# Optimization experiments

Measured on AMD Instinct MI355X. Metric: run time of the kernel, lower is better.

## Reference

```python
import jax, jax.numpy as jnp
import numpy as np

B, D, K = 32768, 256, 2048
BETA = 0.25


def setup_inputs() -> dict:
    key = jax.random.key(0)
    k1, k2 = jax.random.split(key)
    latents = jax.random.normal(k1, (B, D), dtype=jnp.float32)
    # nn.Embedding weight initialized uniform(-1/K, 1/K)
    embedding = jax.random.uniform(k2, (K, D), dtype=jnp.float32,
                                   minval=-1.0 / K, maxval=1.0 / K)
    return {"latents": latents, "embedding": embedding}


def reference(latents, embedding):
    # Squared-L2 distances: [B, K]
    dist = (jnp.sum(latents ** 2, axis=1, keepdims=True)
            + jnp.sum(embedding ** 2, axis=1)
            - 2.0 * jnp.matmul(latents, embedding.T))
    encoding_inds = jnp.argmin(dist, axis=1)  # [B]

    # Gather codebook rows (equivalent to one-hot @ embedding)
    quantized = embedding[encoding_inds]  # [B, D]

    commitment_loss = jnp.mean((jax.lax.stop_gradient(quantized) - latents) ** 2)
    embedding_loss = jnp.mean((quantized - jax.lax.stop_gradient(latents)) ** 2)
    vq_loss = commitment_loss * BETA + embedding_loss

    # Straight-through estimator
    quantized_st = latents + jax.lax.stop_gradient(quantized - latents)

    # avg_probs = mean of one-hot over batch == normalized histogram of inds
    counts = jnp.zeros((K,), dtype=jnp.float32).at[encoding_inds].add(1.0)
    avg_probs = counts / B
    entropy_vq = -jnp.sum(avg_probs * jnp.log(avg_probs + 1e-10))

    # dist values at selected codes
    cluster_metric = jnp.mean(
        jnp.take_along_axis(dist, encoding_inds[:, None], axis=1))

    return (quantized_st, vq_loss, entropy_vq,
            encoding_inds[:, None], cluster_metric)
```

## Files before the change

### kernel.cpp

```cpp
#include <hip/hip_runtime.h>
#include <math.h>

#define B_ROWS 32768
#define D_DIM  256
#define K_CODES 2048

#define OUT_Q   0
#define OUT_VQ  8388608
#define OUT_ENT 8388609
#define OUT_IND 8388610
#define OUT_CM  8421378


#define WS_SE2   0
#define WS_SX2   8192
#define WS_CNT   139264
#define WS_PACK  147456
#define WS_MSEP  409600
#define WS_DISTP 475136
#define WS_BCAT  540672

typedef _Float16 f16x8 __attribute__((ext_vector_type(8)));
typedef float f32x4 __attribute__((ext_vector_type(4)));
typedef union { _Float16 h[4]; uint2 u2; } h4pack;

__global__ __launch_bounds__(256) void k_init(
    const float* __restrict__ X, const float* __restrict__ E,
    _Float16* __restrict__ A, _Float16* __restrict__ Bc,
    float* __restrict__ sx2, float* __restrict__ se2,
    unsigned long long* __restrict__ packed, int* __restrict__ counts) {
  int w = threadIdx.x >> 6, lane = threadIdx.x & 63;
  if (blockIdx.x < 8192) {
    int row = blockIdx.x * 4 + w;
    float4 v = ((const float4*)(X + (size_t)row * D_DIM))[lane];
    float s = v.x * v.x + v.y * v.y + v.z * v.z + v.w * v.w;
#pragma unroll
    for (int off = 32; off > 0; off >>= 1) s += __shfl_xor(s, off, 64);
    if (lane == 0) { sx2[row] = s; packed[row] = ~0ull; }
    h4pack hi, lo;
    hi.h[0] = (_Float16)v.x; hi.h[1] = (_Float16)v.y;
    hi.h[2] = (_Float16)v.z; hi.h[3] = (_Float16)v.w;
    lo.h[0] = (_Float16)((v.x - (float)hi.h[0]) * 4096.0f);
    lo.h[1] = (_Float16)((v.y - (float)hi.h[1]) * 4096.0f);
    lo.h[2] = (_Float16)((v.z - (float)hi.h[2]) * 4096.0f);
    lo.h[3] = (_Float16)((v.w - (float)hi.h[3]) * 4096.0f);
    *(uint2*)&A[(size_t)row * 512 + 4 * lane] = hi.u2;
    *(uint2*)&A[(size_t)row * 512 + 256 + 4 * lane] = lo.u2;
  } else {
    int bb = blockIdx.x - 8192;
    int row = bb * 4 + w;
    if (threadIdx.x < 4) counts[bb * 4 + threadIdx.x] = 0;
    float4 v = ((const float4*)(E + (size_t)row * D_DIM))[lane];
    float s = v.x * v.x + v.y * v.y + v.z * v.z + v.w * v.w;
#pragma unroll
    for (int off = 32; off > 0; off >>= 1) s += __shfl_xor(s, off, 64);
    if (lane == 0) se2[row] = s;
    const float S = 4194304.0f;
    const float SH = 0.000244140625f;
    float e0 = v.x * S, e1 = v.y * S, e2 = v.z * S, e3 = v.w * S;
    h4pack b1, b2, b3;
    b1.h[0] = (_Float16)e0; b1.h[1] = (_Float16)e1;
    b1.h[2] = (_Float16)e2; b1.h[3] = (_Float16)e3;
    b2.h[0] = (_Float16)((float)b1.h[0] * SH);
    b2.h[1] = (_Float16)((float)b1.h[1] * SH);
    b2.h[2] = (_Float16)((float)b1.h[2] * SH);
    b2.h[3] = (_Float16)((float)b1.h[3] * SH);
    b3.h[0] = (_Float16)(e0 - (float)b1.h[0]);
    b3.h[1] = (_Float16)(e1 - (float)b1.h[1]);
    b3.h[2] = (_Float16)(e2 - (float)b1.h[2]);
    b3.h[3] = (_Float16)(e3 - (float)b1.h[3]);
    *(uint2*)&Bc[(size_t)row * 768 + 4 * lane] = b1.u2;
    *(uint2*)&Bc[(size_t)row * 768 + 256 + 4 * lane] = b2.u2;
    *(uint2*)&Bc[(size_t)row * 768 + 512 + 4 * lane] = b3.u2;
  }
}

#define BAR()  __builtin_amdgcn_s_barrier()
#define SB0()  __builtin_amdgcn_sched_barrier(0)
#define WLGKM(n)                                                 \
  do {                                                           \
    asm volatile("s_waitcnt lgkmcnt(" #n ")" ::: "memory");      \
    SB0();                                                       \
  } while (0)
#define DSR(dst, a, o) \
  asm volatile("ds_read_b128 %0, %1 offset:" o : "=v"(dst) : "v"(a))

#define MFMA_QUAD(I0, J0, AF, BF)                                            \
  do {                                                                       \
    __builtin_amdgcn_s_setprio(1);                                           \
    _Pragma("unroll") for (int kk = 0; kk < 2; ++kk) {                       \
      _Pragma("unroll") for (int ii = 0; ii < 4; ++ii) {                     \
        _Pragma("unroll") for (int jj = 0; jj < 2; ++jj) {                   \
          acc[(I0) + ii][(J0) + jj] =                                        \
              __builtin_amdgcn_mfma_f32_16x16x32_f16(                        \
                  (AF)[ii * 2 + kk], (BF)[jj * 2 + kk],                      \
                  acc[(I0) + ii][(J0) + jj], 0, 0, 0);                       \
        }                                                                    \
      }                                                                      \
    }                                                                        \
    __builtin_amdgcn_s_setprio(0);                                           \
  } while (0)

__global__ __launch_bounds__(512, 2) void k_mfma2(
    const _Float16* __restrict__ A, const _Float16* __restrict__ Bc,
    const float* __restrict__ se2, const float* __restrict__ sx2,
    unsigned long long* __restrict__ packed) {
  extern __shared__ char smem[];
  const int tid = threadIdx.x;
  const int w = tid >> 6, lane = tid & 63;
  const int wm = w >> 2, wn = w & 3;
  const int q = lane >> 4, c = lane & 15;
  const int rowb = blockIdx.x & 127, colb = blockIdx.x >> 7;
  const int rowpan = rowb * 256, colpan = colb * 256;
  const int rsel = lane >> 3;
  const int chunkb = ((lane & 7) ^ rsel) * 16;
  const int rswz = c & 7;

  const char* Abase = (const char*)A;
  const char* Bbase = (const char*)Bc;

  auto issue = [&](int tt, int g, int bsel) {
    const int hh = (g == 3 || g == 4 || g == 5 || g == 7) ? 1 : 0;
    const int ss = (g == 2 || g == 4 || g == 6 || g == 7) ? 1 : 0;
    const int rl = hh * 128 + ss * 64 + w * 8 + rsel;
    const char* src;
    char* dst;
    if (g == 0 || g >= 5) {
      int aoff = (tt & 3) * 128 + (((tt >> 2) == 1) ? 512 : 0);
      src = Abase + ((size_t)(rowpan + rl) << 10) + aoff + chunkb;
      dst = smem + bsel * 32768 + hh * 16384 + ss * 8192 + w * 1024;
    } else {
      src = Bbase + (size_t)(colpan + rl) * 1536 + tt * 128 + chunkb;
      dst = smem + 65536 + bsel * 32768 + hh * 16384 + ss * 8192 + w * 1024;
    }
    __builtin_amdgcn_global_load_lds(
        (const __attribute__((address_space(1))) unsigned int*)src,
        (__attribute__((address_space(3))) unsigned int*)dst, 16, 0, 0);
  };

  f32x4 acc[8][4];
#pragma unroll
  for (int i = 0; i < 8; ++i)
#pragma unroll
    for (int j = 0; j < 4; ++j) acc[i][j] = (f32x4){0.f, 0.f, 0.f, 0.f};

  const unsigned ldsA = (unsigned)(uintptr_t)smem + (unsigned)((wm * 128 + c) * 128);
  const unsigned ldsB = (unsigned)(uintptr_t)smem + 65536u +
                        (unsigned)((wn * 64 + c) * 128);
  const unsigned sl0 = (unsigned)(((0 * 4 + q) ^ rswz) * 16);
  const unsigned sl1 = (unsigned)(((1 * 4 + q) ^ rswz) * 16);

#pragma unroll
  for (int g = 0; g < 8; ++g) issue(0, g, 0);
  asm volatile("s_waitcnt vmcnt(0)" ::: "memory");
  BAR();

  f16x8 af[8], bf01[4], bf23[4];

#pragma unroll 2
  for (int t = 0; t < 12; ++t) {
    const int bsel = t & 1;
    const bool pre = (t < 11);
    const unsigned aA0 = ldsA + (unsigned)(bsel * 32768) + sl0;
    const unsigned aA1 = ldsA + (unsigned)(bsel * 32768) + sl1;
    const unsigned aB0 = ldsB + (unsigned)(bsel * 32768) + sl0;
    const unsigned aB1 = ldsB + (unsigned)(bsel * 32768) + sl1;

    if (pre) {
#pragma unroll
      for (int g = 0; g < 8; ++g) issue(t + 1, g, bsel ^ 1);
    }

    DSR(af[0], aA0, "0");    DSR(af[1], aA1, "0");
    DSR(af[2], aA0, "2048"); DSR(af[3], aA1, "2048");
    DSR(af[4], aA0, "4096"); DSR(af[5], aA1, "4096");
    DSR(af[6], aA0, "6144"); DSR(af[7], aA1, "6144");
    DSR(bf01[0], aB0, "0");    DSR(bf01[1], aB1, "0");
    DSR(bf01[2], aB0, "2048"); DSR(bf01[3], aB1, "2048");
    DSR(bf23[0], aB0, "4096"); DSR(bf23[1], aB1, "4096");
    DSR(bf23[2], aB0, "6144"); DSR(bf23[3], aB1, "6144");

    WLGKM(4);
    MFMA_QUAD(0, 0, af, bf01);
    WLGKM(0);
    MFMA_QUAD(0, 2, af, bf23);

    DSR(af[0], aA0, "8192");  DSR(af[1], aA1, "8192");
    DSR(af[2], aA0, "10240"); DSR(af[3], aA1, "10240");
    DSR(af[4], aA0, "12288"); DSR(af[5], aA1, "12288");
    DSR(af[6], aA0, "14336"); DSR(af[7], aA1, "14336");
    WLGKM(0);
    MFMA_QUAD(4, 2, af, bf23);
    MFMA_QUAD(4, 0, af, bf01);

    if (pre) {
      asm volatile("s_waitcnt vmcnt(0)" ::: "memory");
      BAR();
    }
  }

  __syncthreads();

  const float inv = 4.76837158203125e-07f;
  float se_j[4];
#pragma unroll
  for (int j = 0; j < 4; ++j) se_j[j] = se2[colpan + wn * 64 + j * 16 + c];
  unsigned long long* m = (unsigned long long*)smem;
#pragma unroll
  for (int i = 0; i < 8; ++i) {
    float4 sx4 = *(const float4*)&sx2[rowpan + wm * 128 + i * 16 + q * 4];
#pragma unroll
    for (int r = 0; r < 4; ++r) {
      float sx = ((const float*)&sx4)[r];
      float bs = 3.402823466e38f;
      int bk = 0;
#pragma unroll
      for (int j = 0; j < 4; ++j) {
        float t1 = sx + se_j[j];
        float d = t1 - acc[i][j][r] * inv;
        if (d < bs) { bs = d; bk = colpan + wn * 64 + j * 16 + c; }
      }
#pragma unroll
      for (int off = 1; off < 16; off <<= 1) {
        float os = __shfl_xor(bs, off, 64);
        int ok = __shfl_xor(bk, off, 64);
        if (os < bs || (os == bs && ok < bk)) { bs = os; bk = ok; }
      }
      if (c == 0) {
        m[wn * 256 + wm * 128 + i * 16 + q * 4 + r] =
            ((unsigned long long)__float_as_uint(bs) << 32) |
            (unsigned long long)(unsigned int)bk;
      }
    }
  }
  __syncthreads();
  if (tid < 256) {
    unsigned long long v = m[tid];
#pragma unroll
    for (int mm = 1; mm < 4; ++mm) {
      unsigned long long o = m[mm * 256 + tid];
      if (o < v) v = o;
    }
    atomicMin(&packed[rowpan + tid], v);
  }
}

__global__ __launch_bounds__(256) void k_gather(
    const float* __restrict__ X, const float* __restrict__ E,
    const unsigned long long* __restrict__ packed, float* __restrict__ outq,
    float* __restrict__ out_ind, int* __restrict__ counts,
    double* __restrict__ msep, double* __restrict__ distp) {
  __shared__ int sk[16];
  __shared__ float sd[16];
  int tid = threadIdx.x;
  if (tid < 16) {
    int row = blockIdx.x * 16 + tid;
    unsigned long long v = packed[row];
    int k = (int)(v & 0xFFFFFFFFull);
    sk[tid] = k;
    sd[tid] = __uint_as_float((unsigned int)(v >> 32));
    out_ind[row] = (float)k;
    atomicAdd(&counts[k], 1);
  }
  __syncthreads();
  int wave = tid >> 6, lane = tid & 63;
  double msum = 0.0, dsum = 0.0;
#pragma unroll
  for (int rr = 0; rr < 4; rr++) {
    int li = wave * 4 + rr;
    int b = blockIdx.x * 16 + li;
    int ind = sk[li];
    float4 x4 = ((const float4*)(X + (size_t)b * D_DIM))[lane];
    float4 q4 = ((const float4*)(E + (size_t)ind * D_DIM))[lane];
    float d0 = q4.x - x4.x, d1 = q4.y - x4.y, d2 = q4.z - x4.z, d3 = q4.w - x4.w;
    float4 o;
    o.x = x4.x + d0; o.y = x4.y + d1; o.z = x4.z + d2; o.w = x4.w + d3;
    ((float4*)(outq + (size_t)b * D_DIM))[lane] = o;
    float v = d0 * d0 + d1 * d1 + d2 * d2 + d3 * d3;
#pragma unroll
    for (int off = 32; off > 0; off >>= 1) v += __shfl_xor(v, off, 64);
    if (lane == 0) { msum += (double)v; dsum += (double)sd[li]; }
  }
  if (lane == 0) {
    int wg = blockIdx.x * 4 + wave;
    msep[wg] = msum;
    distp[wg] = dsum;
  }
}

__global__ __launch_bounds__(256) void k_final(
    const int* __restrict__ counts, const double* __restrict__ msep,
    const double* __restrict__ distp, float* __restrict__ out) {
  __shared__ double red[256];
  int t = threadIdx.x;

  double m = 0.0;
  for (int i = t; i < 8192; i += 256) m += msep[i];
  red[t] = m;
  __syncthreads();
  for (int s = 128; s > 0; s >>= 1) {
    if (t < s) red[t] += red[t + s];
    __syncthreads();
  }
  if (t == 0) {
    double mse = red[0] / ((double)B_ROWS * (double)D_DIM);
    out[OUT_VQ] = (float)(mse * 1.25);
  }
  __syncthreads();

  double d = 0.0;
  for (int i = t; i < 8192; i += 256) d += distp[i];
  red[t] = d;
  __syncthreads();
  for (int s = 128; s > 0; s >>= 1) {
    if (t < s) red[t] += red[t + s];
    __syncthreads();
  }
  if (t == 0) out[OUT_CM] = (float)(red[0] / (double)B_ROWS);
  __syncthreads();

  double e = 0.0;
  for (int k = t; k < K_CODES; k += 256) {
    float p = (float)counts[k] * (1.0f / 32768.0f);
    e += (double)(p * logf(p + 1e-10f));
  }
  red[t] = e;
  __syncthreads();
  for (int s = 128; s > 0; s >>= 1) {
    if (t < s) red[t] += red[t + s];
    __syncthreads();
  }
  if (t == 0) out[OUT_ENT] = (float)(-red[0]);
}

extern "C" void kernel_launch(void* const* d_in, const int* in_sizes, int n_in,
                              void* d_out, int out_size, void* d_ws,
                              size_t ws_size, hipStream_t stream) {
  const float* X = (const float*)d_in[0];
  const float* E = (const float*)d_in[1];
  float* out = (float*)d_out;
  char* ws = (char*)d_ws;
  float* se2 = (float*)(ws + WS_SE2);
  float* sx2 = (float*)(ws + WS_SX2);
  int* counts = (int*)(ws + WS_CNT);
  unsigned long long* packed = (unsigned long long*)(ws + WS_PACK);
  double* msep = (double*)(ws + WS_MSEP);
  double* distp = (double*)(ws + WS_DISTP);
  _Float16* Bcat = (_Float16*)(ws + WS_BCAT);
  _Float16* Acat = (_Float16*)d_out;

  static bool attr_done = false;
  if (!attr_done) {
    hipFuncSetAttribute((const void*)k_mfma2,
                        hipFuncAttributeMaxDynamicSharedMemorySize, 131072);
    attr_done = true;
  }

  k_init<<<8704, 256, 0, stream>>>(X, E, Acat, Bcat, sx2, se2, packed, counts);
  k_mfma2<<<1024, 512, 131072, stream>>>(Acat, Bcat, se2, sx2, packed);
  k_gather<<<B_ROWS / 16, 256, 0, stream>>>(X, E, packed, out + OUT_Q,
                                            out + OUT_IND, counts, msep, distp);
  k_final<<<1, 256, 0, stream>>>(counts, msep, distp, out);
}
```

Before: 261.2 us.

## Batch row loads in init and gather kernels; drop MFMA priority toggles

The init kernel now has each wave handle four rows and issues all four global loads before any compute, cutting the grid from 8704 to 2176 blocks. The gather kernel likewise hoists all X and codebook-row loads ahead of the arithmetic so more memory requests are in flight at once. Inside the MFMA main loop the s_setprio raises around each MFMA group are removed and sched_barriers are placed between groups, which changes instruction scheduling and wave arbitration. More loads in flight raises register pressure, and dropping the priority hints may change how waves interleave LDS reads and MFMAs.

```diff
diff --git a/kernel.cpp b/kernel.cpp
--- a/kernel.cpp
+++ b/kernel.cpp
@@ -30,48 +30,64 @@
     float* __restrict__ sx2, float* __restrict__ se2,
     unsigned long long* __restrict__ packed, int* __restrict__ counts) {
   int w = threadIdx.x >> 6, lane = threadIdx.x & 63;
-  if (blockIdx.x < 8192) {
-    int row = blockIdx.x * 4 + w;
-    float4 v = ((const float4*)(X + (size_t)row * D_DIM))[lane];
-    float s = v.x * v.x + v.y * v.y + v.z * v.z + v.w * v.w;
-#pragma unroll
-    for (int off = 32; off > 0; off >>= 1) s += __shfl_xor(s, off, 64);
-    if (lane == 0) { sx2[row] = s; packed[row] = ~0ull; }
-    h4pack hi, lo;
-    hi.h[0] = (_Float16)v.x; hi.h[1] = (_Float16)v.y;
-    hi.h[2] = (_Float16)v.z; hi.h[3] = (_Float16)v.w;
-    lo.h[0] = (_Float16)((v.x - (float)hi.h[0]) * 4096.0f);
-    lo.h[1] = (_Float16)((v.y - (float)hi.h[1]) * 4096.0f);
-    lo.h[2] = (_Float16)((v.z - (float)hi.h[2]) * 4096.0f);
-    lo.h[3] = (_Float16)((v.w - (float)hi.h[3]) * 4096.0f);
-    *(uint2*)&A[(size_t)row * 512 + 4 * lane] = hi.u2;
-    *(uint2*)&A[(size_t)row * 512 + 256 + 4 * lane] = lo.u2;
+  if (blockIdx.x < 2048) {
+    int row0 = blockIdx.x * 16 + w * 4;
+    float4 v4[4];
+#pragma unroll
+    for (int r = 0; r < 4; ++r)
+      v4[r] = ((const float4*)(X + (size_t)(row0 + r) * D_DIM))[lane];
+#pragma unroll
+    for (int r = 0; r < 4; ++r) {
+      int row = row0 + r;
+      float4 v = v4[r];
+      float s = v.x * v.x + v.y * v.y + v.z * v.z + v.w * v.w;
+#pragma unroll
+      for (int off = 32; off > 0; off >>= 1) s += __shfl_xor(s, off, 64);
+      if (lane == 0) { sx2[row] = s; packed[row] = ~0ull; }
+      h4pack hi, lo;
+      hi.h[0] = (_Float16)v.x; hi.h[1] = (_Float16)v.y;
+      hi.h[2] = (_Float16)v.z; hi.h[3] = (_Float16)v.w;
+      lo.h[0] = (_Float16)((v.x - (float)hi.h[0]) * 4096.0f);
+      lo.h[1] = (_Float16)((v.y - (float)hi.h[1]) * 4096.0f);
+      lo.h[2] = (_Float16)((v.z - (float)hi.h[2]) * 4096.0f);
+      lo.h[3] = (_Float16)((v.w - (float)hi.h[3]) * 4096.0f);
+      *(uint2*)&A[(size_t)row * 512 + 4 * lane] = hi.u2;
+      *(uint2*)&A[(size_t)row * 512 + 256 + 4 * lane] = lo.u2;
+    }
   } else {
-    int bb = blockIdx.x - 8192;
-    int row = bb * 4 + w;
-    if (threadIdx.x < 4) counts[bb * 4 + threadIdx.x] = 0;
-    float4 v = ((const float4*)(E + (size_t)row * D_DIM))[lane];
-    float s = v.x * v.x + v.y * v.y + v.z * v.z + v.w * v.w;
-#pragma unroll
-    for (int off = 32; off > 0; off >>= 1) s += __shfl_xor(s, off, 64);
-    if (lane == 0) se2[row] = s;
+    int eb = blockIdx.x - 2048;
+    int row0 = eb * 16 + w * 4;
+    if (threadIdx.x < 16) counts[eb * 16 + threadIdx.x] = 0;
+    float4 v4[4];
+#pragma unroll
+    for (int r = 0; r < 4; ++r)
+      v4[r] = ((const float4*)(E + (size_t)(row0 + r) * D_DIM))[lane];
     const float S = 4194304.0f;
     const float SH = 0.000244140625f;
-    float e0 = v.x * S, e1 = v.y * S, e2 = v.z * S, e3 = v.w * S;
-    h4pack b1, b2, b3;
-    b1.h[0] = (_Float16)e0; b1.h[1] = (_Float16)e1;
-    b1.h[2] = (_Float16)e2; b1.h[3] = (_Float16)e3;
-    b2.h[0] = (_Float16)((float)b1.h[0] * SH);
-    b2.h[1] = (_Float16)((float)b1.h[1] * SH);
-    b2.h[2] = (_Float16)((float)b1.h[2] * SH);
-    b2.h[3] = (_Float16)((float)b1.h[3] * SH);
-    b3.h[0] = (_Float16)(e0 - (float)b1.h[0]);
-    b3.h[1] = (_Float16)(e1 - (float)b1.h[1]);
-    b3.h[2] = (_Float16)(e2 - (float)b1.h[2]);
-    b3.h[3] = (_Float16)(e3 - (float)b1.h[3]);
-    *(uint2*)&Bc[(size_t)row * 768 + 4 * lane] = b1.u2;
-    *(uint2*)&Bc[(size_t)row * 768 + 256 + 4 * lane] = b2.u2;
-    *(uint2*)&Bc[(size_t)row * 768 + 512 + 4 * lane] = b3.u2;
+#pragma unroll
+    for (int r = 0; r < 4; ++r) {
+      int row = row0 + r;
+      float4 v = v4[r];
+      float s = v.x * v.x + v.y * v.y + v.z * v.z + v.w * v.w;
+#pragma unroll
+      for (int off = 32; off > 0; off >>= 1) s += __shfl_xor(s, off, 64);
+      if (lane == 0) se2[row] = s;
+      float e0 = v.x * S, e1 = v.y * S, e2 = v.z * S, e3 = v.w * S;
+      h4pack b1, b2, b3;
+      b1.h[0] = (_Float16)e0; b1.h[1] = (_Float16)e1;
+      b1.h[2] = (_Float16)e2; b1.h[3] = (_Float16)e3;
+      b2.h[0] = (_Float16)((float)b1.h[0] * SH);
+      b2.h[1] = (_Float16)((float)b1.h[1] * SH);
+      b2.h[2] = (_Float16)((float)b1.h[2] * SH);
+      b2.h[3] = (_Float16)((float)b1.h[3] * SH);
+      b3.h[0] = (_Float16)(e0 - (float)b1.h[0]);
+      b3.h[1] = (_Float16)(e1 - (float)b1.h[1]);
+      b3.h[2] = (_Float16)(e2 - (float)b1.h[2]);
+      b3.h[3] = (_Float16)(e3 - (float)b1.h[3]);
+      *(uint2*)&Bc[(size_t)row * 768 + 4 * lane] = b1.u2;
+      *(uint2*)&Bc[(size_t)row * 768 + 256 + 4 * lane] = b2.u2;
+      *(uint2*)&Bc[(size_t)row * 768 + 512 + 4 * lane] = b3.u2;
+    }
   }
 }
 
@@ -87,7 +103,6 @@
 
 #define MFMA_QUAD(I0, J0, AF, BF)                                            \
   do {                                                                       \
-    __builtin_amdgcn_s_setprio(1);                                           \
     _Pragma("unroll") for (int kk = 0; kk < 2; ++kk) {                       \
       _Pragma("unroll") for (int ii = 0; ii < 4; ++ii) {                     \
         _Pragma("unroll") for (int jj = 0; jj < 2; ++jj) {                   \
@@ -98,7 +113,6 @@
         }                                                                    \
       }                                                                      \
     }                                                                        \
-    __builtin_amdgcn_s_setprio(0);                                           \
   } while (0)
 
 __global__ __launch_bounds__(512, 2) void k_mfma2(
@@ -182,8 +196,10 @@
 
     WLGKM(4);
     MFMA_QUAD(0, 0, af, bf01);
+    SB0();
     WLGKM(0);
     MFMA_QUAD(0, 2, af, bf23);
+    SB0();
 
     DSR(af[0], aA0, "8192");  DSR(af[1], aA1, "8192");
     DSR(af[2], aA0, "10240"); DSR(af[3], aA1, "10240");
@@ -191,7 +207,9 @@
     DSR(af[6], aA0, "14336"); DSR(af[7], aA1, "14336");
     WLGKM(0);
     MFMA_QUAD(4, 2, af, bf23);
+    SB0();
     MFMA_QUAD(4, 0, af, bf01);
+    SB0();
 
     if (pre) {
       asm volatile("s_waitcnt vmcnt(0)" ::: "memory");
@@ -264,14 +282,19 @@
   }
   __syncthreads();
   int wave = tid >> 6, lane = tid & 63;
+  float4 x4v[4], q4v[4];
+#pragma unroll
+  for (int rr = 0; rr < 4; rr++) {
+    int b = blockIdx.x * 16 + wave * 4 + rr;
+    x4v[rr] = ((const float4*)(X + (size_t)b * D_DIM))[lane];
+    q4v[rr] = ((const float4*)(E + (size_t)sk[wave * 4 + rr] * D_DIM))[lane];
+  }
   double msum = 0.0, dsum = 0.0;
 #pragma unroll
   for (int rr = 0; rr < 4; rr++) {
     int li = wave * 4 + rr;
     int b = blockIdx.x * 16 + li;
-    int ind = sk[li];
-    float4 x4 = ((const float4*)(X + (size_t)b * D_DIM))[lane];
-    float4 q4 = ((const float4*)(E + (size_t)ind * D_DIM))[lane];
+    float4 x4 = x4v[rr], q4 = q4v[rr];
     float d0 = q4.x - x4.x, d1 = q4.y - x4.y, d2 = q4.z - x4.z, d3 = q4.w - x4.w;
     float4 o;
     o.x = x4.x + d0; o.y = x4.y + d1; o.z = x4.z + d2; o.w = x4.w + d3;
@@ -356,7 +379,7 @@
     attr_done = true;
   }
 
-  k_init<<<8704, 256, 0, stream>>>(X, E, Acat, Bcat, sx2, se2, packed, counts);
+  k_init<<<2176, 256, 0, stream>>>(X, E, Acat, Bcat, sx2, se2, packed, counts);
   k_mfma2<<<1024, 512, 131072, stream>>>(Acat, Bcat, se2, sx2, packed);
   k_gather<<<B_ROWS / 16, 256, 0, stream>>>(X, E, packed, out + OUT_Q,
                                             out + OUT_IND, counts, msep, distp);
```

New measurement: 262.4 us. No clear change (+0.5%).
